# Optimization experiments

Hardware: AMD Instinct MI355X
Metric: run time of the kernel (lower is better)

The kernel has to match this reference:

```python
import jax, jax.numpy as jnp
import numpy as np

B, D, H = 64, 512, 8
EPS = 1e-8


def setup_inputs() -> dict:
    key = jax.random.key(0)
    k1, k2, k3 = jax.random.split(key, 3)
    x = jax.random.normal(k1, (B, D), dtype=jnp.float32)
    # alphas/betas: one scalar per (head, transform); columns = (query, key, value)
    alphas = jax.random.uniform(k2, (H, 3), dtype=jnp.float32)
    betas = jax.random.uniform(k3, (H, 3), dtype=jnp.float32)
    return {"x": x, "alphas": alphas, "betas": betas}


def reference(x, alphas, betas):
    # x: [B, D]; alphas, betas: [H, 3] (query, key, value scalar affine params per head)
    d = x.shape[-1]
    # qkv[h, t, b, d] = alphas[h, t] * x[b, d] + betas[h, t]  (ones vector -> plain bias)
    qkv = alphas[:, :, None, None] * x[None, None, :, :] + betas[:, :, None, None]  # [H,3,B,D]
    q, k, v = qkv[:, 0], qkv[:, 1], qkv[:, 2]  # each [H, B, D]
    # diff[h,b,i,j] = |q[h,b,j] - k[h,b,i]|  (row i = key feature, col j = query feature)
    diff = jnp.abs(q[:, :, None, :] - k[:, :, :, None]) + EPS  # [H, B, D, D]
    sim = jax.nn.softmax(1.0 / diff, axis=-1) / jnp.sqrt(jnp.float32(d))
    # attended[h,b,i] = sum_j sim[h,b,i,j] * v[h,b,j]  (batched matvec)
    attended = jnp.einsum("hbij,hbj->hbi", sim, v)  # [H, B, D]
    return x + attended.sum(axis=0)
```

## Files before the change

### kernel.cpp

```cpp
#include <hip/hip_runtime.h>
#include <math.h>

#define BB 64
#define DD 512
#define HH 8
#define EPS 1e-8f

__device__ __forceinline__ float fast_rcp(float d) {
    return __builtin_amdgcn_rcpf(d);
}

__global__ __launch_bounds__(512, 8) void flattn_kernel(
    const float* __restrict__ x,
    const float* __restrict__ alphas,
    const float* __restrict__ betas,
    float* __restrict__ out)
{
    const int b  = blockIdx.x;
    const int ic = blockIdx.y;
    const int h  = blockIdx.z;

    __shared__ float xs[DD];
    __shared__ float mind_sh[2][256];
    __shared__ float ss_sh[256];
    __shared__ float sx_sh[256];

    const int tid = threadIdx.x;
    const int ii  = tid & 255;
    const int jc  = tid >> 8;
    const int i   = ic * 256 + ii;

    const float a0 = alphas[h * 3 + 0];
    const float a1 = alphas[h * 3 + 1];
    const float a2 = alphas[h * 3 + 2];
    const float b0 = betas[h * 3 + 0];
    const float b1 = betas[h * 3 + 1];
    const float b2 = betas[h * 3 + 2];

    xs[tid] = x[b * DD + tid];
    __syncthreads();

    const float xi = xs[i];
    const float c  = b0 - fmaf(a1, xi, b1);

    const int j0 = jc * 256;

    float mind = 3.0e38f;
    #pragma unroll 4
    for (int j = j0; j < j0 + 256; j += 4) {
        float4 x4 = *(const float4*)&xs[j];
        mind = fminf(mind, fabsf(fmaf(a0, x4.x, c)));
        mind = fminf(mind, fabsf(fmaf(a0, x4.y, c)));
        mind = fminf(mind, fabsf(fmaf(a0, x4.z, c)));
        mind = fminf(mind, fabsf(fmaf(a0, x4.w, c)));
    }
    mind_sh[jc][ii] = mind;
    __syncthreads();

    mind = fminf(mind_sh[0][ii], mind_sh[1][ii]);
    const float m = fast_rcp(mind + EPS);
    const float log2e = 1.4426950408889634f;
    const float negml = -m * log2e;

    float ss = 0.0f, sx = 0.0f;
    #pragma unroll 2
    for (int j = j0; j < j0 + 256; j += 4) {
        float4 x4 = *(const float4*)&xs[j];
        {
            float t = fmaf(a0, x4.x, c);
            float r = fast_rcp(fabsf(t) + EPS);
            float s = __builtin_amdgcn_exp2f(fmaf(r, log2e, negml));
            ss += s; sx = fmaf(s, x4.x, sx);
        }
        {
            float t = fmaf(a0, x4.y, c);
            float r = fast_rcp(fabsf(t) + EPS);
            float s = __builtin_amdgcn_exp2f(fmaf(r, log2e, negml));
            ss += s; sx = fmaf(s, x4.y, sx);
        }
        {
            float t = fmaf(a0, x4.z, c);
            float r = fast_rcp(fabsf(t) + EPS);
            float s = __builtin_amdgcn_exp2f(fmaf(r, log2e, negml));
            ss += s; sx = fmaf(s, x4.z, sx);
        }
        {
            float t = fmaf(a0, x4.w, c);
            float r = fast_rcp(fabsf(t) + EPS);
            float s = __builtin_amdgcn_exp2f(fmaf(r, log2e, negml));
            ss += s; sx = fmaf(s, x4.w, sx);
        }
    }

    if (jc == 1) { ss_sh[ii] = ss; sx_sh[ii] = sx; }
    __syncthreads();
    if (jc == 0) {
        ss += ss_sh[ii];
        sx += sx_sh[ii];
        const float scale = 0.04419417382415922f;
        float sv  = fmaf(a2, sx, b2 * ss);
        float att = sv * fast_rcp(ss) * scale;
        if (h == 0) att += xi;
        atomicAdd(&out[b * DD + i], att);
    }
}

extern "C" void kernel_launch(void* const* d_in, const int* in_sizes, int n_in,
                              void* d_out, int out_size, void* d_ws, size_t ws_size,
                              hipStream_t stream) {
    const float* x      = (const float*)d_in[0];
    const float* alphas = (const float*)d_in[1];
    const float* betas  = (const float*)d_in[2];
    float* out = (float*)d_out;

    hipMemsetAsync(out, 0, (size_t)out_size * sizeof(float), stream);

    dim3 grid(BB, 2, HH);
    dim3 block(512);
    flattn_kernel<<<grid, block, 0, stream>>>(x, alphas, betas, out);
}
```

Baseline: 92.03 us.

## Sort rows and skip chunks with negligible softmax weight

Adds a rank-based sort kernel that orders each row of x, so the attention kernel works on sorted features with chunks of similar values. Per-chunk minimum distances are recorded, and whole 32-element chunks are skipped wave-wide when every lane's exponent falls more than about 28 below the max, where terms underflow or become negligible. This removes most of the rcp/exp work in the softmax pass. The cost is an extra launch, workspace traffic and an index gather for the output scatter, plus a small approximation from dropping tiny terms.

```diff
diff --git a/kernel.cpp b/kernel.cpp
--- a/kernel.cpp
+++ b/kernel.cpp
@@ -5,13 +5,39 @@
 #define DD 512
 #define HH 8
 #define EPS 1e-8f
+#define NCH 8
+#define CS 32
 
 __device__ __forceinline__ float fast_rcp(float d) {
     return __builtin_amdgcn_rcpf(d);
 }
 
+__global__ __launch_bounds__(512) void sort_rows(
+    const float* __restrict__ x,
+    float* __restrict__ xsorted,
+    unsigned short* __restrict__ isorted)
+{
+    const int b = blockIdx.x;
+    const int i = threadIdx.x;
+    __shared__ float sx[DD];
+    const float xi = x[b * DD + i];
+    sx[i] = xi;
+    __syncthreads();
+    int rank = 0;
+    for (int j = 0; j < DD; j += 4) {
+        float4 v = *(const float4*)&sx[j];
+        rank += (v.x < xi) | ((v.x == xi) & ((j + 0) < i));
+        rank += (v.y < xi) | ((v.y == xi) & ((j + 1) < i));
+        rank += (v.z < xi) | ((v.z == xi) & ((j + 2) < i));
+        rank += (v.w < xi) | ((v.w == xi) & ((j + 3) < i));
+    }
+    xsorted[b * DD + rank] = xi;
+    isorted[b * DD + rank] = (unsigned short)i;
+}
+
 __global__ __launch_bounds__(512, 8) void flattn_kernel(
-    const float* __restrict__ x,
+    const float* __restrict__ xsorted,
+    const unsigned short* __restrict__ isorted,
     const float* __restrict__ alphas,
     const float* __restrict__ betas,
     float* __restrict__ out)
@@ -37,58 +63,73 @@
     const float b1 = betas[h * 3 + 1];
     const float b2 = betas[h * 3 + 2];
 
-    xs[tid] = x[b * DD + tid];
+    xs[tid] = xsorted[b * DD + tid];
     __syncthreads();
 
     const float xi = xs[i];
     const float c  = b0 - fmaf(a1, xi, b1);
-
     const int j0 = jc * 256;
 
-    float mind = 3.0e38f;
-    #pragma unroll 4
-    for (int j = j0; j < j0 + 256; j += 4) {
-        float4 x4 = *(const float4*)&xs[j];
-        mind = fminf(mind, fabsf(fmaf(a0, x4.x, c)));
-        mind = fminf(mind, fabsf(fmaf(a0, x4.y, c)));
-        mind = fminf(mind, fabsf(fmaf(a0, x4.z, c)));
-        mind = fminf(mind, fabsf(fmaf(a0, x4.w, c)));
+    float cmin[NCH];
+    float gmin = 3.0e38f;
+    #pragma unroll
+    for (int ch = 0; ch < NCH; ++ch) {
+        const int base = j0 + ch * CS;
+        float cm = 3.0e38f;
+        #pragma unroll
+        for (int jj = 0; jj < CS; jj += 4) {
+            float4 x4 = *(const float4*)&xs[base + jj];
+            cm = fminf(cm, fabsf(fmaf(a0, x4.x, c)));
+            cm = fminf(cm, fabsf(fmaf(a0, x4.y, c)));
+            cm = fminf(cm, fabsf(fmaf(a0, x4.z, c)));
+            cm = fminf(cm, fabsf(fmaf(a0, x4.w, c)));
+        }
+        cmin[ch] = cm;
+        gmin = fminf(gmin, cm);
     }
-    mind_sh[jc][ii] = mind;
+    mind_sh[jc][ii] = gmin;
     __syncthreads();
 
-    mind = fminf(mind_sh[0][ii], mind_sh[1][ii]);
-    const float m = fast_rcp(mind + EPS);
+    gmin = fminf(mind_sh[0][ii], mind_sh[1][ii]);
+    const float m = fast_rcp(gmin + EPS);
     const float log2e = 1.4426950408889634f;
     const float negml = -m * log2e;
+    const float mr = m - 28.0f;
+    const float thr = (mr > 0.0f) ? fast_rcp(mr) : 3.0e38f;
 
     float ss = 0.0f, sx = 0.0f;
-    #pragma unroll 2
-    for (int j = j0; j < j0 + 256; j += 4) {
-        float4 x4 = *(const float4*)&xs[j];
-        {
-            float t = fmaf(a0, x4.x, c);
-            float r = fast_rcp(fabsf(t) + EPS);
-            float s = __builtin_amdgcn_exp2f(fmaf(r, log2e, negml));
-            ss += s; sx = fmaf(s, x4.x, sx);
-        }
-        {
-            float t = fmaf(a0, x4.y, c);
-            float r = fast_rcp(fabsf(t) + EPS);
-            float s = __builtin_amdgcn_exp2f(fmaf(r, log2e, negml));
-            ss += s; sx = fmaf(s, x4.y, sx);
-        }
-        {
-            float t = fmaf(a0, x4.z, c);
-            float r = fast_rcp(fabsf(t) + EPS);
-            float s = __builtin_amdgcn_exp2f(fmaf(r, log2e, negml));
-            ss += s; sx = fmaf(s, x4.z, sx);
-        }
-        {
-            float t = fmaf(a0, x4.w, c);
-            float r = fast_rcp(fabsf(t) + EPS);
-            float s = __builtin_amdgcn_exp2f(fmaf(r, log2e, negml));
-            ss += s; sx = fmaf(s, x4.w, sx);
+    #pragma unroll
+    for (int ch = 0; ch < NCH; ++ch) {
+        if (__ballot(cmin[ch] <= thr)) {
+            const int base = j0 + ch * CS;
+            #pragma unroll 4
+            for (int jj = 0; jj < CS; jj += 4) {
+                float4 x4 = *(const float4*)&xs[base + jj];
+                {
+                    float t = fmaf(a0, x4.x, c);
+                    float r = fast_rcp(fabsf(t) + EPS);
+                    float s = __builtin_amdgcn_exp2f(fmaf(r, log2e, negml));
+                    ss += s; sx = fmaf(s, x4.x, sx);
+                }
+                {
+                    float t = fmaf(a0, x4.y, c);
+                    float r = fast_rcp(fabsf(t) + EPS);
+                    float s = __builtin_amdgcn_exp2f(fmaf(r, log2e, negml));
+                    ss += s; sx = fmaf(s, x4.y, sx);
+                }
+                {
+                    float t = fmaf(a0, x4.z, c);
+                    float r = fast_rcp(fabsf(t) + EPS);
+                    float s = __builtin_amdgcn_exp2f(fmaf(r, log2e, negml));
+                    ss += s; sx = fmaf(s, x4.z, sx);
+                }
+                {
+                    float t = fmaf(a0, x4.w, c);
+                    float r = fast_rcp(fabsf(t) + EPS);
+                    float s = __builtin_amdgcn_exp2f(fmaf(r, log2e, negml));
+                    ss += s; sx = fmaf(s, x4.w, sx);
+                }
+            }
         }
     }
 
@@ -101,7 +142,8 @@
         float sv  = fmaf(a2, sx, b2 * ss);
         float att = sv * fast_rcp(ss) * scale;
         if (h == 0) att += xi;
-        atomicAdd(&out[b * DD + i], att);
+        const int oi = (int)isorted[b * DD + i];
+        atomicAdd(&out[b * DD + oi], att);
     }
 }
 
@@ -113,9 +155,14 @@
     const float* betas  = (const float*)d_in[2];
     float* out = (float*)d_out;
 
+    float* xsorted = (float*)d_ws;
+    unsigned short* isorted = (unsigned short*)(xsorted + BB * DD);
+
     hipMemsetAsync(out, 0, (size_t)out_size * sizeof(float), stream);
+
+    sort_rows<<<dim3(BB), dim3(DD), 0, stream>>>(x, xsorted, isorted);
 
     dim3 grid(BB, 2, HH);
     dim3 block(512);
-    flattn_kernel<<<grid, block, 0, stream>>>(x, alphas, betas, out);
+    flattn_kernel<<<grid, block, 0, stream>>>(xsorted, isorted, alphas, betas, out);
 }
```

New measurement: 98.62 us. 7.2% more time.

## Sort features per row and skip negligible softmax chunks, fuse heads per block

Applied to the files above, without the earlier changes.

Each block now sorts its row of x by rank counting, so a thread's 32-wide chunk of j values is contiguous in value. For each chunk it computes a partial minimum distance and skips the exp/rcp pass when that chunk's contribution falls below a threshold derived from the row max (m-28 margin). All 8 heads are processed in one block of 1024 threads and summed in shared memory, which removes the atomicAdd and the memset. The cost is a quadratic rank sort per block, extra barriers, and a large shared-memory footprint. Outputs are approximate only in the skipped exp terms, which underflow to negligible values.

```diff
diff --git a/kernel.cpp b/kernel.cpp
--- a/kernel.cpp
+++ b/kernel.cpp
@@ -1,5 +1,6 @@
 #include <hip/hip_runtime.h>
 #include <math.h>
+#include <stdint.h>
 
 #define BB 64
 #define DD 512
@@ -10,7 +11,7 @@
     return __builtin_amdgcn_rcpf(d);
 }
 
-__global__ __launch_bounds__(512, 8) void flattn_kernel(
+__global__ __launch_bounds__(1024, 8) void flattn_kernel(
     const float* __restrict__ x,
     const float* __restrict__ alphas,
     const float* __restrict__ betas,
@@ -18,90 +19,154 @@
 {
     const int b  = blockIdx.x;
     const int ic = blockIdx.y;
-    const int h  = blockIdx.z;
 
     __shared__ float xs[DD];
-    __shared__ float mind_sh[2][256];
-    __shared__ float ss_sh[256];
-    __shared__ float sx_sh[256];
+    __shared__ int   idxs[DD];
+    __shared__ float attp[HH][64];
+    __shared__ union {
+        struct { uint64_t keys[DD]; int cnt[2][DD]; } s;
+        struct { float pmin[4][16][64], pss[4][16][64], psx[4][16][64]; } g;
+    } u;
 
     const int tid = threadIdx.x;
-    const int ii  = tid & 255;
-    const int jc  = tid >> 8;
-    const int i   = ic * 256 + ii;
 
-    const float a0 = alphas[h * 3 + 0];
-    const float a1 = alphas[h * 3 + 1];
-    const float a2 = alphas[h * 3 + 2];
-    const float b0 = betas[h * 3 + 0];
-    const float b1 = betas[h * 3 + 1];
-    const float b2 = betas[h * 3 + 2];
-
-    xs[tid] = x[b * DD + tid];
+    const int si = tid & (DD - 1);
+    const int sg = tid >> 9;
+    const float xv = x[b * DD + si];
+    if (sg == 0) {
+        uint32_t w = __float_as_uint(xv);
+        uint32_t k = (w & 0x80000000u) ? ~w : (w | 0x80000000u);
+        u.s.keys[si] = ((uint64_t)k << 32) | (uint32_t)si;
+    }
+    __syncthreads();
+    {
+        const uint64_t myk = u.s.keys[si];
+        const int jb = sg * 256;
+        int rk = 0;
+        #pragma unroll 8
+        for (int j = jb; j < jb + 256; j += 2) {
+            rk += (u.s.keys[j]     < myk);
+            rk += (u.s.keys[j + 1] < myk);
+        }
+        u.s.cnt[sg][si] = rk;
+    }
+    __syncthreads();
+    if (sg == 0) {
+        const int rank = u.s.cnt[0][si] + u.s.cnt[1][si];
+        xs[rank]   = xv;
+        idxs[rank] = si;
+    }
     __syncthreads();
 
+    const int ii = tid & 63;
+    const int jc = tid >> 6;
+    const int i  = ic * 64 + ii;
+    const int jb = jc * 32;
     const float xi = xs[i];
-    const float c  = b0 - fmaf(a1, xi, b1);
 
-    const int j0 = jc * 256;
+    const float scale = 0.04419417382415922f;
+    const float log2e = 1.4426950408889634f;
 
-    float mind = 3.0e38f;
-    #pragma unroll 4
-    for (int j = j0; j < j0 + 256; j += 4) {
-        float4 x4 = *(const float4*)&xs[j];
-        mind = fminf(mind, fabsf(fmaf(a0, x4.x, c)));
-        mind = fminf(mind, fabsf(fmaf(a0, x4.y, c)));
-        mind = fminf(mind, fabsf(fmaf(a0, x4.z, c)));
-        mind = fminf(mind, fabsf(fmaf(a0, x4.w, c)));
-    }
-    mind_sh[jc][ii] = mind;
-    __syncthreads();
+    for (int gset = 0; gset < 2; ++gset) {
+        float a0v[4], c[4], cm[4];
+        #pragma unroll
+        for (int hh = 0; hh < 4; ++hh) {
+            const int h = gset * 4 + hh;
+            a0v[hh] = alphas[h * 3 + 0];
+            const float a1 = alphas[h * 3 + 1];
+            c[hh]  = betas[h * 3 + 0] - fmaf(a1, xi, betas[h * 3 + 1]);
+            cm[hh] = 3.0e38f;
+        }
 
-    mind = fminf(mind_sh[0][ii], mind_sh[1][ii]);
-    const float m = fast_rcp(mind + EPS);
-    const float log2e = 1.4426950408889634f;
-    const float negml = -m * log2e;
+        #pragma unroll
+        for (int jj = 0; jj < 32; jj += 4) {
+            float4 x4 = *(const float4*)&xs[jb + jj];
+            #pragma unroll
+            for (int hh = 0; hh < 4; ++hh) {
+                float ta = fmaf(a0v[hh], x4.x, c[hh]), tb = fmaf(a0v[hh], x4.y, c[hh]);
+                float tc = fmaf(a0v[hh], x4.z, c[hh]), td = fmaf(a0v[hh], x4.w, c[hh]);
+                cm[hh] = fminf(cm[hh], fminf(fabsf(ta), fabsf(tb)));
+                cm[hh] = fminf(cm[hh], fminf(fabsf(tc), fabsf(td)));
+            }
+        }
+        #pragma unroll
+        for (int hh = 0; hh < 4; ++hh) u.g.pmin[hh][jc][ii] = cm[hh];
+        __syncthreads();
 
-    float ss = 0.0f, sx = 0.0f;
-    #pragma unroll 2
-    for (int j = j0; j < j0 + 256; j += 4) {
-        float4 x4 = *(const float4*)&xs[j];
-        {
-            float t = fmaf(a0, x4.x, c);
-            float r = fast_rcp(fabsf(t) + EPS);
-            float s = __builtin_amdgcn_exp2f(fmaf(r, log2e, negml));
-            ss += s; sx = fmaf(s, x4.x, sx);
+        float ssv[4], sxv[4];
+        #pragma unroll
+        for (int hh = 0; hh < 4; ++hh) {
+            float gm = 3.0e38f;
+            #pragma unroll
+            for (int k = 0; k < 16; ++k) gm = fminf(gm, u.g.pmin[hh][k][ii]);
+            const float m = fast_rcp(gm + EPS);
+            const float negml = -m * log2e;
+            const float mr = m - 28.0f;
+            const float thr = (mr > 0.0f) ? fast_rcp(mr) : 3.0e38f;
+
+            float ss = 0.0f, sx = 0.0f;
+            if (__ballot(cm[hh] <= thr)) {
+                const float a0 = a0v[hh], cc = c[hh];
+                #pragma unroll
+                for (int jj = 0; jj < 32; jj += 4) {
+                    float4 x4 = *(const float4*)&xs[jb + jj];
+                    {
+                        float t = fmaf(a0, x4.x, cc);
+                        float r = fast_rcp(fabsf(t) + EPS);
+                        float s = __builtin_amdgcn_exp2f(fmaf(r, log2e, negml));
+                        ss += s; sx = fmaf(s, x4.x, sx);
+                    }
+                    {
+                        float t = fmaf(a0, x4.y, cc);
+                        float r = fast_rcp(fabsf(t) + EPS);
+                        float s = __builtin_amdgcn_exp2f(fmaf(r, log2e, negml));
+                        ss += s; sx = fmaf(s, x4.y, sx);
+                    }
+                    {
+                        float t = fmaf(a0, x4.z, cc);
+                        float r = fast_rcp(fabsf(t) + EPS);
+                        float s = __builtin_amdgcn_exp2f(fmaf(r, log2e, negml));
+                        ss += s; sx = fmaf(s, x4.z, sx);
+                    }
+                    {
+                        float t = fmaf(a0, x4.w, cc);
+                        float r = fast_rcp(fabsf(t) + EPS);
+                        float s = __builtin_amdgcn_exp2f(fmaf(r, log2e, negml));
+                        ss += s; sx = fmaf(s, x4.w, sx);
+                    }
+                }
+            }
+            ssv[hh] = ss; sxv[hh] = sx;
         }
-        {
-            float t = fmaf(a0, x4.y, c);
-            float r = fast_rcp(fabsf(t) + EPS);
-            float s = __builtin_amdgcn_exp2f(fmaf(r, log2e, negml));
-            ss += s; sx = fmaf(s, x4.y, sx);
+        #pragma unroll
+        for (int hh = 0; hh < 4; ++hh) {
+            u.g.pss[hh][jc][ii] = ssv[hh];
+            u.g.psx[hh][jc][ii] = sxv[hh];
         }
-        {
-            float t = fmaf(a0, x4.z, c);
-            float r = fast_rcp(fabsf(t) + EPS);
-            float s = __builtin_amdgcn_exp2f(fmaf(r, log2e, negml));
-            ss += s; sx = fmaf(s, x4.z, sx);
+        __syncthreads();
+
+        if (jc < 4) {
+            const int hh = jc;
+            const int h  = gset * 4 + hh;
+            float ss = 0.0f, sx = 0.0f;
+            #pragma unroll
+            for (int k = 0; k < 16; ++k) {
+                ss += u.g.pss[hh][k][ii];
+                sx += u.g.psx[hh][k][ii];
+            }
+            const float a2 = alphas[h * 3 + 2];
+            const float b2 = betas[h * 3 + 2];
+            float sv = fmaf(a2, sx, b2 * ss);
+            attp[h][ii] = sv * fast_rcp(ss) * scale;
         }
-        {
-            float t = fmaf(a0, x4.w, c);
-            float r = fast_rcp(fabsf(t) + EPS);
-            float s = __builtin_amdgcn_exp2f(fmaf(r, log2e, negml));
-            ss += s; sx = fmaf(s, x4.w, sx);
-        }
+        __syncthreads();
     }
 
-    if (jc == 1) { ss_sh[ii] = ss; sx_sh[ii] = sx; }
-    __syncthreads();
-    if (jc == 0) {
-        ss += ss_sh[ii];
-        sx += sx_sh[ii];
-        const float scale = 0.04419417382415922f;
-        float sv  = fmaf(a2, sx, b2 * ss);
-        float att = sv * fast_rcp(ss) * scale;
-        if (h == 0) att += xi;
-        atomicAdd(&out[b * DD + i], att);
+    if (tid < 64) {
+        float acc = xs[ic * 64 + tid];
+        #pragma unroll
+        for (int h = 0; h < HH; ++h) acc += attp[h][tid];
+        out[b * DD + idxs[ic * 64 + tid]] = acc;
     }
 }
 
@@ -113,9 +178,7 @@
     const float* betas  = (const float*)d_in[2];
     float* out = (float*)d_out;
 
-    hipMemsetAsync(out, 0, (size_t)out_size * sizeof(float), stream);
-
-    dim3 grid(BB, 2, HH);
-    dim3 block(512);
+    dim3 grid(BB, DD / 64);
+    dim3 block(1024);
     flattn_kernel<<<grid, block, 0, stream>>>(x, alphas, betas, out);
 }
```

Measured after the change: 93.56 us. No clear change (+1.7%).
